# Kernel tuning notes

Measured on AMD Instinct MI355X. Metric: run time of the kernel, lower is better.

Reference implementation:

```python
import jax, jax.numpy as jnp
import numpy as np


def setup_inputs() -> dict:
    key = jax.random.key(0)
    k1, k2 = jax.random.split(key)
    B, C, H, W = 8, 64, 32, 32
    K = 8192
    x = jax.random.normal(k1, (B, C, H, W), dtype=jnp.float32)
    codebook = jax.random.normal(k2, (K, C), dtype=jnp.float32)
    return {"x": x, "codebook": codebook}


def reference(x, codebook):
    """Faithful JAX version of VQVAE.quantize().

    x:        [B, C, H, W] latent (output of pre_quant_conv)
    codebook: [K, C] embedding weight
    Returns (quant_out [B,C,H,W], commitment_loss, codebook_loss, indices [B,H,W]).
    """
    B, C, H, W = x.shape
    # [B, H, W, C] -> [B, N, C]
    xf = jnp.transpose(x, (0, 2, 3, 1)).reshape(B, H * W, C)

    # Squared pairwise distances (argmin of cdist == argmin of squared dist).
    x2 = jnp.sum(xf * xf, axis=-1, keepdims=True)            # [B, N, 1]
    e2 = jnp.sum(codebook * codebook, axis=-1)               # [K]
    xe = jnp.einsum('bnc,kc->bnk', xf, codebook)             # [B, N, K]
    d2 = x2 + e2[None, None, :] - 2.0 * xe                   # [B, N, K]
    idx = jnp.argmin(d2, axis=-1)                            # [B, N]

    quant = codebook[idx.reshape(-1)]                        # [B*N, C]
    xflat = xf.reshape(-1, C)                                # [B*N, C]

    commitment_loss = jnp.mean((jax.lax.stop_gradient(quant) - xflat) ** 2)
    codebook_loss = jnp.mean((quant - jax.lax.stop_gradient(xflat)) ** 2)

    # Straight-through estimator.
    quant_st = xflat + jax.lax.stop_gradient(quant - xflat)
    quant_out = jnp.transpose(quant_st.reshape(B, H, W, C), (0, 3, 1, 2))
    indices = idx.reshape(B, H, W)
    return quant_out, commitment_loss, codebook_loss, indices
```

## Files before the change

### kernel.cpp

```cpp
#include <hip/hip_runtime.h>


#define N_PTS   8192
#define K_CODES 8192
#define C_DIM   64
#define HWSZ    1024
#define QOUT_N  524288
#define SPLITS  32

#define WS_XS    0
#define WS_CBS   2097152
#define WS_E2H   4194304
#define WS_PACK  4227072
#define WS_PART  6324224

typedef __attribute__((ext_vector_type(8))) short    short8;
typedef __attribute__((ext_vector_type(8))) _Float16 half8;
typedef __attribute__((ext_vector_type(4))) float    floatx4;

__device__ __forceinline__ half8 as_h8(short8 v) {
    return __builtin_bit_cast(half8, v);
}
__device__ __forceinline__ void split2(float v, unsigned short& h,
                                       unsigned short& m) {
    _Float16 hh = (_Float16)v;
    float r = v - (float)hh;
    _Float16 mm = (_Float16)r;
    h = __builtin_bit_cast(unsigned short, hh);
    m = __builtin_bit_cast(unsigned short, mm);
}
__device__ __forceinline__ void cp16(const void* g, void* l) {
    __builtin_amdgcn_global_load_lds(
        (const __attribute__((address_space(1))) void*)g,
        (__attribute__((address_space(3))) void*)l, 16, 0, 0);
}
__device__ __forceinline__ void cp4(const void* g, void* l) {
    __builtin_amdgcn_global_load_lds(
        (const __attribute__((address_space(1))) void*)g,
        (__attribute__((address_space(3))) void*)l, 4, 0, 0);
}

__global__ __launch_bounds__(256)
void vq_prep_kernel(const float* __restrict__ x,
                    const float* __restrict__ cb,
                    unsigned short* __restrict__ xS,
                    unsigned short* __restrict__ cbS,
                    float* __restrict__ e2h)
{
    const int bx  = blockIdx.x;
    const int tid = threadIdx.x;

    if (bx < 32) {
        const int k = bx * 256 + tid;
        const float* row = cb + k * C_DIM;
        float s = 0.0f;
        #pragma unroll
        for (int g = 0; g < 8; ++g) {
            float4 a = *(const float4*)(row + g * 8);
            float4 b = *(const float4*)(row + g * 8 + 4);
            float vv[8] = {a.x, a.y, a.z, a.w, b.x, b.y, b.z, b.w};
            unsigned short h8[8], m8[8];
            #pragma unroll
            for (int j = 0; j < 8; ++j) {
                s = fmaf(vv[j], vv[j], s);
                split2(vv[j], h8[j], m8[j]);
            }
            *(uint4*)(cbS + ((size_t)(0 * 8 + g) * 8192 + k) * 8) = *(const uint4*)h8;
            *(uint4*)(cbS + ((size_t)(1 * 8 + g) * 8192 + k) * 8) = *(const uint4*)m8;
        }
        e2h[k] = 0.5f * s;
    } else {
        const int u = bx - 32;
        const int b = u >> 3, g = u & 7;
        const float* xb = x + (size_t)(b * C_DIM + g * 8) * HWSZ;
        float v[4][8];
        #pragma unroll
        for (int cq = 0; cq < 8; ++cq) {
            float4 t4 = *(const float4*)(xb + cq * HWSZ + tid * 4);
            v[0][cq] = t4.x; v[1][cq] = t4.y; v[2][cq] = t4.z; v[3][cq] = t4.w;
        }
        #pragma unroll
        for (int j = 0; j < 4; ++j) {
            unsigned short h8[8], m8[8];
            #pragma unroll
            for (int cq = 0; cq < 8; ++cq)
                split2(v[j][cq], h8[cq], m8[cq]);
            const size_t n = (size_t)b * 1024 + tid * 4 + j;
            *(uint4*)(xS + ((size_t)(0 * 8 + g) * 8192 + n) * 8) = *(const uint4*)h8;
            *(uint4*)(xS + ((size_t)(1 * 8 + g) * 8192 + n) * 8) = *(const uint4*)m8;
        }
    }
}

#define SEG_SHORTS 512
#define NSEGS      16
#define BUF_SHORTS 8320

__device__ __forceinline__ void computeTile(const half8 af[4][2][2],
                                            const unsigned short* __restrict__ bsrc,
                                            int tl, int quad, int col, int code,
                                            float bestv[4][4], int besti[4][4])
{
    half8 bf[2][2];
    #pragma unroll
    for (int p = 0; p < 2; ++p)
        #pragma unroll
        for (int s = 0; s < 2; ++s) {
            int seg = p * 8 + s * 4 + quad;
            bf[p][s] = as_h8(*(const short8*)(bsrc + seg * SEG_SHORTS + (tl * 16 + col) * 8));
        }
    float me2 = -((const float*)(bsrc + NSEGS * SEG_SHORTS))[tl * 16 + col];

    floatx4 acc[4];
    #pragma unroll
    for (int t = 0; t < 4; ++t) acc[t] = (floatx4){me2, me2, me2, me2};

    #pragma unroll
    for (int s = 0; s < 2; ++s) {
        #pragma unroll
        for (int t = 0; t < 4; ++t)
            acc[t] = __builtin_amdgcn_mfma_f32_16x16x32_f16(af[t][0][s], bf[0][s], acc[t], 0, 0, 0);
        #pragma unroll
        for (int t = 0; t < 4; ++t)
            acc[t] = __builtin_amdgcn_mfma_f32_16x16x32_f16(af[t][0][s], bf[1][s], acc[t], 0, 0, 0);
        #pragma unroll
        for (int t = 0; t < 4; ++t)
            acc[t] = __builtin_amdgcn_mfma_f32_16x16x32_f16(af[t][1][s], bf[0][s], acc[t], 0, 0, 0);
    }

    #pragma unroll
    for (int t = 0; t < 4; ++t)
        #pragma unroll
        for (int r = 0; r < 4; ++r) {
            float sc = acc[t][r];
            bool gt = sc > bestv[t][r];
            bestv[t][r] = gt ? sc   : bestv[t][r];
            besti[t][r] = gt ? code : besti[t][r];
        }
}

__global__ __launch_bounds__(256, 2)
void vq_argmin_kernel(const unsigned short* __restrict__ xS,
                      const unsigned short* __restrict__ cbS,
                      const float* __restrict__ e2h,
                      unsigned long long* __restrict__ packedS)
{
    __shared__ __align__(16) unsigned short sBuf[2][BUF_SHORTS];

    const int tid   = threadIdx.x;
    const int lane  = tid & 63;
    const int w     = tid >> 6;
    const int col   = lane & 15;
    const int quad  = lane >> 4;
    const int mb    = blockIdx.x;
    const int split = blockIdx.y;
    const int m0    = mb * 256 + w * 64;
    const int nb0   = split * 256;

    half8 af[4][2][2];
    #pragma unroll
    for (int t = 0; t < 4; ++t) {
        int pt = m0 + t * 16 + col;
        #pragma unroll
        for (int p = 0; p < 2; ++p)
            #pragma unroll
            for (int s = 0; s < 2; ++s) {
                int g = s * 4 + quad;
                af[t][p][s] = as_h8(*(const short8*)(xS + ((size_t)(p * 8 + g) * 8192 + pt) * 8));
            }
    }

    float bestv[4][4];
    int   besti[4][4];
    #pragma unroll
    for (int t = 0; t < 4; ++t)
        #pragma unroll
        for (int r = 0; r < 4; ++r) {
            bestv[t][r] = __uint_as_float(0xFF800000u);
            besti[t][r] = 0;
        }

    auto stage = [&](int k0, int buf) {
        unsigned short* dst = &sBuf[buf][0];
        #pragma unroll
        for (int i = 0; i < 4; ++i) {
            int f   = tid + i * 256;
            int seg = f >> 6;
            int l   = f & 63;
            cp16(cbS + ((size_t)seg * 8192 + k0 + l) * 8,
                 dst + seg * SEG_SHORTS + l * 8);
        }
        if (tid < 64)
            cp4(e2h + k0 + tid, (float*)(dst + NSEGS * SEG_SHORTS) + tid);
    };

    stage(nb0, 0);
    __syncthreads();

    for (int ch = 0; ch < 4; ++ch) {
        if (ch + 1 < 4) stage(nb0 + (ch + 1) * 64, (ch + 1) & 1);
        const unsigned short* bsrc = &sBuf[ch & 1][0];
        #pragma unroll
        for (int tl = 0; tl < 4; ++tl)
            computeTile(af, bsrc, tl, quad, col,
                        nb0 + ch * 64 + tl * 16 + col, bestv, besti);
        __syncthreads();
    }

    unsigned long long own = 0;
    #pragma unroll
    for (int t = 0; t < 4; ++t)
        #pragma unroll
        for (int r = 0; r < 4; ++r) {
            unsigned u = __float_as_uint(-bestv[t][r]);
            u = ((int)u < 0) ? ~u : (u | 0x80000000u);
            unsigned long long p = ((unsigned long long)u << 32) | (unsigned)besti[t][r];
            #pragma unroll
            for (int msk = 1; msk < 16; msk <<= 1) {
                unsigned long long q = __shfl_xor(p, msk, 64);
                p = (q < p) ? q : p;
            }
            own = (col == t * 4 + r) ? p : own;
        }
    const int mpt = m0 + (col >> 2) * 16 + quad * 4 + (col & 3);
    packedS[(size_t)split * N_PTS + mpt] = own;
}

__global__ __launch_bounds__(256)
void vq_gather_kernel(const float* __restrict__ x,
                      const float* __restrict__ cb,
                      const unsigned long long* __restrict__ packedS,
                      float* __restrict__ out,
                      float* __restrict__ part)
{
    __shared__ unsigned long long sred[4][64];
    const int tid  = threadIdx.x;
    const int lane = tid & 63;
    const int qd   = tid >> 6;
    const int n0   = blockIdx.x * 64;
    const int n    = n0 + lane;

    {
        unsigned long long v = packedS[(size_t)(qd * 8) * N_PTS + n];
        #pragma unroll
        for (int s = 1; s < 8; ++s) {
            unsigned long long q = packedS[(size_t)(qd * 8 + s) * N_PTS + n];
            v = (q < v) ? q : v;
        }
        sred[qd][lane] = v;
    }
    __syncthreads();

    unsigned long long v = sred[0][lane];
    #pragma unroll
    for (int s = 1; s < 4; ++s) {
        unsigned long long q = sred[s][lane];
        v = (q < v) ? q : v;
    }
    const int idx = (int)(v & 0xFFFFFFFFull);
    if (qd == 0) out[QOUT_N + 2 + n] = (float)idx;

    const int c0  = qd * 16;
    const int b   = n >> 10;
    const int hw  = n & 1023;
    const float* xb = x   + (size_t)b * (C_DIM * HWSZ) + hw;
    float*       ob = out + (size_t)b * (C_DIM * HWSZ) + hw;

    float s = 0.0f;
    #pragma unroll
    for (int c4 = 0; c4 < 4; ++c4) {
        float4 q = *(const float4*)(cb + (size_t)idx * C_DIM + c0 + c4 * 4);
        float qa[4] = {q.x, q.y, q.z, q.w};
        #pragma unroll
        for (int j = 0; j < 4; ++j) {
            int c = c0 + c4 * 4 + j;
            float xv = xb[c * HWSZ];
            float d  = qa[j] - xv;
            s = fmaf(d, d, s);
            ob[c * HWSZ] = xv + d;
        }
    }

    #pragma unroll
    for (int off = 32; off > 0; off >>= 1) s += __shfl_down(s, off, 64);
    if (lane == 0) part[blockIdx.x * 4 + qd] = s;
}

__global__ __launch_bounds__(256)
void vq_final_kernel(const float* __restrict__ part, float* __restrict__ out)
{
    __shared__ float w[4];
    float s = part[threadIdx.x] + part[threadIdx.x + 256];
    #pragma unroll
    for (int off = 32; off > 0; off >>= 1) s += __shfl_down(s, off, 64);
    if ((threadIdx.x & 63) == 0) w[threadIdx.x >> 6] = s;
    __syncthreads();
    if (threadIdx.x == 0) {
        float m = (w[0] + w[1] + w[2] + w[3]) * (1.0f / (float)QOUT_N);
        out[QOUT_N]     = m;
        out[QOUT_N + 1] = m;
    }
}

extern "C" void kernel_launch(void* const* d_in, const int* in_sizes, int n_in,
                              void* d_out, int out_size, void* d_ws, size_t ws_size,
                              hipStream_t stream)
{
    const float* x  = (const float*)d_in[0];
    const float* cb = (const float*)d_in[1];
    float* out = (float*)d_out;
    char*  ws  = (char*)d_ws;
    (void)ws_size;

    unsigned short* xS  = (unsigned short*)(ws + WS_XS);
    unsigned short* cbS = (unsigned short*)(ws + WS_CBS);
    float* e2h = (float*)(ws + WS_E2H);
    unsigned long long* packedS = (unsigned long long*)(ws + WS_PACK);
    float* part = (float*)(ws + WS_PART);

    vq_prep_kernel<<<96, 256, 0, stream>>>(x, cb, xS, cbS, e2h);
    vq_argmin_kernel<<<dim3(N_PTS / 256, SPLITS), 256, 0, stream>>>(xS, cbS, e2h, packedS);
    vq_gather_kernel<<<128, 256, 0, stream>>>(x, cb, packedS, out, part);
    vq_final_kernel<<<1, 256, 0, stream>>>(part, out);
}
```

Before: 94.26 us.

## Switch argmin to 32x32x16 MFMA tiles and fold loss reduction into atomics

Recasts the distance GEMM from 16x16x32 MFMA tiles over 64 points per wave to 32x32x16 MFMA tiles over 32 points per wave. The grid doubles along the point dimension to 64x32 blocks, and the cross-lane argmin shuffle now spans 32 lanes. Separately, the final loss reduction kernel is removed: each gather wave atomically adds its scaled partial sum into the output, and the prep kernel zeroes those two slots. This saves one kernel launch, at the cost of nondeterministic float summation order and less A-operand reuse per wave, since each codebook tile loaded from LDS is now used against fewer points.

After: 114.9 us. 21.9% more time.

```diff
diff --git a/kernel.cpp b/kernel.cpp
--- a/kernel.cpp
+++ b/kernel.cpp
@@ -12,11 +12,10 @@
 #define WS_CBS   2097152
 #define WS_E2H   4194304
 #define WS_PACK  4227072
-#define WS_PART  6324224
-
-typedef __attribute__((ext_vector_type(8))) short    short8;
-typedef __attribute__((ext_vector_type(8))) _Float16 half8;
-typedef __attribute__((ext_vector_type(4))) float    floatx4;
+
+typedef __attribute__((ext_vector_type(8)))  short    short8;
+typedef __attribute__((ext_vector_type(8)))  _Float16 half8;
+typedef __attribute__((ext_vector_type(16))) float    floatx16;
 
 __device__ __forceinline__ half8 as_h8(short8 v) {
     return __builtin_bit_cast(half8, v);
@@ -45,10 +44,16 @@
                     const float* __restrict__ cb,
                     unsigned short* __restrict__ xS,
                     unsigned short* __restrict__ cbS,
-                    float* __restrict__ e2h)
+                    float* __restrict__ e2h,
+                    float* __restrict__ out)
 {
     const int bx  = blockIdx.x;
     const int tid = threadIdx.x;
+
+    if (bx == 0 && tid == 0) {
+        out[QOUT_N]     = 0.0f;
+        out[QOUT_N + 1] = 0.0f;
+    }
 
     if (bx < 32) {
         const int k = bx * 256 + tid;
@@ -96,47 +101,35 @@
 #define NSEGS      16
 #define BUF_SHORTS 8320
 
-__device__ __forceinline__ void computeTile(const half8 af[4][2][2],
-                                            const unsigned short* __restrict__ bsrc,
-                                            int tl, int quad, int col, int code,
-                                            float bestv[4][4], int besti[4][4])
-{
-    half8 bf[2][2];
-    #pragma unroll
-    for (int p = 0; p < 2; ++p)
-        #pragma unroll
-        for (int s = 0; s < 2; ++s) {
-            int seg = p * 8 + s * 4 + quad;
-            bf[p][s] = as_h8(*(const short8*)(bsrc + seg * SEG_SHORTS + (tl * 16 + col) * 8));
-        }
-    float me2 = -((const float*)(bsrc + NSEGS * SEG_SHORTS))[tl * 16 + col];
-
-    floatx4 acc[4];
-    #pragma unroll
-    for (int t = 0; t < 4; ++t) acc[t] = (floatx4){me2, me2, me2, me2};
-
-    #pragma unroll
-    for (int s = 0; s < 2; ++s) {
-        #pragma unroll
-        for (int t = 0; t < 4; ++t)
-            acc[t] = __builtin_amdgcn_mfma_f32_16x16x32_f16(af[t][0][s], bf[0][s], acc[t], 0, 0, 0);
-        #pragma unroll
-        for (int t = 0; t < 4; ++t)
-            acc[t] = __builtin_amdgcn_mfma_f32_16x16x32_f16(af[t][0][s], bf[1][s], acc[t], 0, 0, 0);
-        #pragma unroll
-        for (int t = 0; t < 4; ++t)
-            acc[t] = __builtin_amdgcn_mfma_f32_16x16x32_f16(af[t][1][s], bf[0][s], acc[t], 0, 0, 0);
-    }
-
-    #pragma unroll
-    for (int t = 0; t < 4; ++t)
-        #pragma unroll
-        for (int r = 0; r < 4; ++r) {
-            float sc = acc[t][r];
-            bool gt = sc > bestv[t][r];
-            bestv[t][r] = gt ? sc   : bestv[t][r];
-            besti[t][r] = gt ? code : besti[t][r];
-        }
+__device__ __forceinline__ void computeTile32(const half8 af[2][4],
+                                              const unsigned short* __restrict__ bsrc,
+                                              int nt, int l31, int half, int code,
+                                              float bestv[16], int besti[16])
+{
+    const int lc = nt * 32 + l31;
+    const float me2 = -((const float*)(bsrc + NSEGS * SEG_SHORTS))[lc];
+
+    floatx16 acc;
+    #pragma unroll
+    for (int r = 0; r < 16; ++r) acc[r] = me2;
+
+    #pragma unroll
+    for (int s = 0; s < 4; ++s) {
+        const int g = s * 2 + half;
+        half8 bh = as_h8(*(const short8*)(bsrc + (0 * 8 + g) * SEG_SHORTS + lc * 8));
+        half8 bm = as_h8(*(const short8*)(bsrc + (1 * 8 + g) * SEG_SHORTS + lc * 8));
+        acc = __builtin_amdgcn_mfma_f32_32x32x16_f16(af[0][s], bh, acc, 0, 0, 0);
+        acc = __builtin_amdgcn_mfma_f32_32x32x16_f16(af[1][s], bh, acc, 0, 0, 0);
+        acc = __builtin_amdgcn_mfma_f32_32x32x16_f16(af[0][s], bm, acc, 0, 0, 0);
+    }
+
+    #pragma unroll
+    for (int r = 0; r < 16; ++r) {
+        float sc = acc[r];
+        bool gt = sc > bestv[r];
+        bestv[r] = gt ? sc   : bestv[r];
+        besti[r] = gt ? code : besti[r];
+    }
 }
 
 __global__ __launch_bounds__(256, 2)
@@ -150,35 +143,32 @@
     const int tid   = threadIdx.x;
     const int lane  = tid & 63;
     const int w     = tid >> 6;
-    const int col   = lane & 15;
-    const int quad  = lane >> 4;
+    const int l31   = lane & 31;
+    const int half  = lane >> 5;
     const int mb    = blockIdx.x;
     const int split = blockIdx.y;
-    const int m0    = mb * 256 + w * 64;
+    const int m0    = mb * 128 + w * 32;
     const int nb0   = split * 256;
 
-    half8 af[4][2][2];
-    #pragma unroll
-    for (int t = 0; t < 4; ++t) {
-        int pt = m0 + t * 16 + col;
+    half8 af[2][4];
+    {
+        const int pt = m0 + l31;
         #pragma unroll
         for (int p = 0; p < 2; ++p)
             #pragma unroll
-            for (int s = 0; s < 2; ++s) {
-                int g = s * 4 + quad;
-                af[t][p][s] = as_h8(*(const short8*)(xS + ((size_t)(p * 8 + g) * 8192 + pt) * 8));
+            for (int s = 0; s < 4; ++s) {
+                int g = s * 2 + half;
+                af[p][s] = as_h8(*(const short8*)(xS + ((size_t)(p * 8 + g) * 8192 + pt) * 8));
             }
     }
 
-    float bestv[4][4];
-    int   besti[4][4];
-    #pragma unroll
-    for (int t = 0; t < 4; ++t)
-        #pragma unroll
-        for (int r = 0; r < 4; ++r) {
-            bestv[t][r] = __uint_as_float(0xFF800000u);
-            besti[t][r] = 0;
-        }
+    float bestv[16];
+    int   besti[16];
+    #pragma unroll
+    for (int r = 0; r < 16; ++r) {
+        bestv[r] = __uint_as_float(0xFF800000u);
+        besti[r] = 0;
+    }
 
     auto stage = [&](int k0, int buf) {
         unsigned short* dst = &sBuf[buf][0];
@@ -200,38 +190,35 @@
     for (int ch = 0; ch < 4; ++ch) {
         if (ch + 1 < 4) stage(nb0 + (ch + 1) * 64, (ch + 1) & 1);
         const unsigned short* bsrc = &sBuf[ch & 1][0];
-        #pragma unroll
-        for (int tl = 0; tl < 4; ++tl)
-            computeTile(af, bsrc, tl, quad, col,
-                        nb0 + ch * 64 + tl * 16 + col, bestv, besti);
+        computeTile32(af, bsrc, 0, l31, half, nb0 + ch * 64 + l31,      bestv, besti);
+        computeTile32(af, bsrc, 1, l31, half, nb0 + ch * 64 + 32 + l31, bestv, besti);
         __syncthreads();
     }
 
     unsigned long long own = 0;
     #pragma unroll
-    for (int t = 0; t < 4; ++t)
-        #pragma unroll
-        for (int r = 0; r < 4; ++r) {
-            unsigned u = __float_as_uint(-bestv[t][r]);
-            u = ((int)u < 0) ? ~u : (u | 0x80000000u);
-            unsigned long long p = ((unsigned long long)u << 32) | (unsigned)besti[t][r];
-            #pragma unroll
-            for (int msk = 1; msk < 16; msk <<= 1) {
-                unsigned long long q = __shfl_xor(p, msk, 64);
-                p = (q < p) ? q : p;
-            }
-            own = (col == t * 4 + r) ? p : own;
-        }
-    const int mpt = m0 + (col >> 2) * 16 + quad * 4 + (col & 3);
-    packedS[(size_t)split * N_PTS + mpt] = own;
+    for (int r = 0; r < 16; ++r) {
+        unsigned u = __float_as_uint(-bestv[r]);
+        u = ((int)u < 0) ? ~u : (u | 0x80000000u);
+        unsigned long long p = ((unsigned long long)u << 32) | (unsigned)besti[r];
+        #pragma unroll
+        for (int msk = 1; msk < 32; msk <<= 1) {
+            unsigned long long q = __shfl_xor(p, msk, 64);
+            p = (q < p) ? q : p;
+        }
+        own = (l31 == r) ? p : own;
+    }
+    if (l31 < 16) {
+        const int row = (l31 & 3) + 8 * (l31 >> 2) + 4 * half;
+        packedS[(size_t)split * N_PTS + m0 + row] = own;
+    }
 }
 
 __global__ __launch_bounds__(256)
 void vq_gather_kernel(const float* __restrict__ x,
                       const float* __restrict__ cb,
                       const unsigned long long* __restrict__ packedS,
-                      float* __restrict__ out,
-                      float* __restrict__ part)
+                      float* __restrict__ out)
 {
     __shared__ unsigned long long sred[4][64];
     const int tid  = threadIdx.x;
@@ -283,22 +270,10 @@
 
     #pragma unroll
     for (int off = 32; off > 0; off >>= 1) s += __shfl_down(s, off, 64);
-    if (lane == 0) part[blockIdx.x * 4 + qd] = s;
-}
-
-__global__ __launch_bounds__(256)
-void vq_final_kernel(const float* __restrict__ part, float* __restrict__ out)
-{
-    __shared__ float w[4];
-    float s = part[threadIdx.x] + part[threadIdx.x + 256];
-    #pragma unroll
-    for (int off = 32; off > 0; off >>= 1) s += __shfl_down(s, off, 64);
-    if ((threadIdx.x & 63) == 0) w[threadIdx.x >> 6] = s;
-    __syncthreads();
-    if (threadIdx.x == 0) {
-        float m = (w[0] + w[1] + w[2] + w[3]) * (1.0f / (float)QOUT_N);
-        out[QOUT_N]     = m;
-        out[QOUT_N + 1] = m;
+    if (lane == 0) {
+        float m = s * (1.0f / (float)QOUT_N);
+        atomicAdd(out + QOUT_N,     m);
+        atomicAdd(out + QOUT_N + 1, m);
     }
 }
 
@@ -316,10 +291,8 @@
     unsigned short* cbS = (unsigned short*)(ws + WS_CBS);
     float* e2h = (float*)(ws + WS_E2H);
     unsigned long long* packedS = (unsigned long long*)(ws + WS_PACK);
-    float* part = (float*)(ws + WS_PART);
-
-    vq_prep_kernel<<<96, 256, 0, stream>>>(x, cb, xS, cbS, e2h);
-    vq_argmin_kernel<<<dim3(N_PTS / 256, SPLITS), 256, 0, stream>>>(xS, cbS, e2h, packedS);
-    vq_gather_kernel<<<128, 256, 0, stream>>>(x, cb, packedS, out, part);
-    vq_final_kernel<<<1, 256, 0, stream>>>(part, out);
-}
+
+    vq_prep_kernel<<<96, 256, 0, stream>>>(x, cb, xS, cbS, e2h, out);
+    vq_argmin_kernel<<<dim3(64, SPLITS), 256, 0, stream>>>(xS, cbS, e2h, packedS);
+    vq_gather_kernel<<<128, 256, 0, stream>>>(x, cb, packedS, out);
+}
```
